# Optimization experiments

Measured on AMD Instinct MI355X. Metric: run time of the kernel, lower is better.

Reference implementation:

```python
import jax, jax.numpy as jnp
import numpy as np

HID = 512
BATCH = 64
SRC_LEN = 2048


def setup_inputs() -> dict:
    key = jax.random.key(0)
    ks = jax.random.split(key, 8)
    s = 1.0 / np.sqrt(HID)
    return {
        "h": jax.random.normal(ks[0], (1, BATCH, HID), dtype=jnp.float32),
        "enc_out": jax.random.normal(ks[1], (BATCH, SRC_LEN, HID), dtype=jnp.float32),
        "W1_w": jax.random.uniform(ks[2], (HID, HID), jnp.float32, -s, s),
        "W1_b": jax.random.uniform(ks[3], (HID,), jnp.float32, -s, s),
        "W2_w": jax.random.uniform(ks[4], (HID, HID), jnp.float32, -s, s),
        "W2_b": jax.random.uniform(ks[5], (HID,), jnp.float32, -s, s),
        "V_w": jax.random.uniform(ks[6], (1, HID), jnp.float32, -s, s),
        "V_b": jax.random.uniform(ks[7], (1,), jnp.float32, -s, s),
    }


def reference(h, enc_out, W1_w, W1_b, W2_w, W2_b, V_w, V_b):
    # h: [1, B, H] -> [B, 1, H]; broadcast against enc_out: [B, S, H]
    h_b = jnp.transpose(h, (1, 0, 2))                       # [B, 1, H]
    proj_enc = jnp.einsum('bsh,oh->bso', enc_out, W1_w) + W1_b  # [B, S, H]
    proj_h = jnp.einsum('bqh,oh->bqo', h_b, W2_w) + W2_b        # [B, 1, H]
    energy = jnp.tanh(proj_enc + proj_h)                        # [B, S, H]
    scores = jnp.einsum('bsh,oh->bso', energy, V_w)[..., 0] + V_b[0]  # [B, S]
    return jax.nn.softmax(scores, axis=1)
```

## Files before the change

kernel.cpp:

```cpp
#include <hip/hip_runtime.h>
#include <hip/hip_bf16.h>

#define HID   512
#define BATCH 64
#define SRC   2048
#define MROWS (BATCH * SRC)

typedef __bf16 bf16x8 __attribute__((ext_vector_type(8)));
typedef __bf16 bf16x4 __attribute__((ext_vector_type(4)));
typedef float  f32x16 __attribute__((ext_vector_type(16)));

#define PANEL 520

__device__ inline float fast_tanh(float x) {
    float e = __builtin_amdgcn_exp2f(x * 2.8853900817779268f);
    return 1.0f - 2.0f * __builtin_amdgcn_rcpf(e + 1.0f);
}

template <int CTRL>
__device__ inline float dpp_add(float x) {
    int y = __builtin_amdgcn_update_dpp(0, __builtin_bit_cast(int, x), CTRL, 0xF, 0xF, true);
    return x + __builtin_bit_cast(float, y);
}

__device__ inline float reduce32(float x) {
    x = dpp_add<0xB1>(x);
    x = dpp_add<0x4E>(x);
    x = dpp_add<0x141>(x);
    x = dpp_add<0x140>(x);
    int y = __builtin_amdgcn_ds_swizzle(__builtin_bit_cast(int, x), 0x401F);
    return x + __builtin_bit_cast(float, y);
}

__global__ void prep(const float* __restrict__ W1w, __bf16* __restrict__ Bpk,
                     const float* __restrict__ h, const float* __restrict__ W2w,
                     const float* __restrict__ W2b, const float* __restrict__ W1b,
                     float* __restrict__ biasc) {
    __shared__ float hh[HID];
    int tid = threadIdx.x;
    if (blockIdx.x < 128) {
        int t = blockIdx.x * 256 + tid;
        int l = t & 63, tile = t >> 6;
        int ot = tile & 15, kt = tile >> 4;
        int o = ot * 32 + (l & 31);
        int k = kt * 16 + (l >> 5) * 8;
        const float* src = W1w + (size_t)o * HID + k;
        float4 v0 = *(const float4*)src;
        float4 v1 = *(const float4*)(src + 4);
        bf16x8 r;
        r[0]=(__bf16)v0.x; r[1]=(__bf16)v0.y; r[2]=(__bf16)v0.z; r[3]=(__bf16)v0.w;
        r[4]=(__bf16)v1.x; r[5]=(__bf16)v1.y; r[6]=(__bf16)v1.z; r[7]=(__bf16)v1.w;
        ((bf16x8*)Bpk)[t] = r;
    } else {
        int b = blockIdx.x - 128;
        hh[tid]       = h[b * HID + tid];
        hh[tid + 256] = h[b * HID + tid + 256];
        __syncthreads();
        const float4* h4 = (const float4*)hh;
        for (int o = tid; o < HID; o += 256) {
            const float4* w4 = (const float4*)(W2w + (size_t)o * HID);
            float s = 0.f;
            #pragma unroll 8
            for (int k = 0; k < HID / 4; ++k) {
                float4 a = h4[k]; float4 w = w4[k];
                s += a.x * w.x + a.y * w.y + a.z * w.z + a.w * w.w;
            }
            biasc[b * HID + o] = s + W2b[o] + W1b[o];
        }
    }
}

__global__ __launch_bounds__(512, 4) void attn_main(
        const float* __restrict__ enc, const __bf16* __restrict__ Bpk,
        const float* __restrict__ biasc, const float* __restrict__ Vw,
        float* __restrict__ scores) {
    __shared__ __bf16 AL[64 * PANEL];
    __shared__ float sred[64][9];

    const int tid = threadIdx.x;
    const int blockRow = blockIdx.x * 64;
    const int b = blockIdx.x >> 5;
    const int lane = tid & 63;
    const int wv = tid >> 6;
    const int col = lane & 31;
    const int hfi = lane >> 5;

    const int o0 = (2 * wv) * 32 + col;
    const int o1 = o0 + 32;
    float bb0 = biasc[b * HID + o0], bb1 = biasc[b * HID + o1];
    float vv0 = Vw[o0],               vv1 = Vw[o1];

    const float4* encB = (const float4*)enc + (size_t)blockRow * 128;
    #pragma unroll
    for (int i = 0; i < 16; ++i) {
        int f = i * 512 + tid;
        float4 v = encB[f];
        int row = f >> 7;
        int kq  = (f & 127) << 2;
        int kt = kq >> 4, half = (kq >> 3) & 1, j = kq & 7;
        int off = (kt * 2 + (row >> 5)) * PANEL + ((row & 31) + 32 * half) * 8 + j;
        bf16x4 o4;
        o4[0]=(__bf16)v.x; o4[1]=(__bf16)v.y; o4[2]=(__bf16)v.z; o4[3]=(__bf16)v.w;
        *(bf16x4*)&AL[off] = o4;
    }
    __syncthreads();

    const int rot = blockIdx.x & 31;
    const char* BpkB = (const char*)Bpk + (2 * wv) * 1024 + lane * 16;
    const __bf16* pA = AL + lane * 8;

    f32x16 acc00, acc01, acc10, acc11;
    #pragma unroll
    for (int i = 0; i < 16; ++i) { acc00[i]=0.f; acc01[i]=0.f; acc10[i]=0.f; acc11[i]=0.f; }

    bf16x8 b0 = *(const bf16x8*)(BpkB + (size_t)rot * 16384);
    bf16x8 b1 = *(const bf16x8*)(BpkB + (size_t)rot * 16384 + 1024);
    #pragma unroll 8
    for (int kt = 0; kt < 32; ++kt) {
        int in = (kt + 1 + rot) & 31;
        bf16x8 nb0 = *(const bf16x8*)(BpkB + (size_t)in * 16384);
        bf16x8 nb1 = *(const bf16x8*)(BpkB + (size_t)in * 16384 + 1024);
        int ia = (kt + rot) & 31;
        const __bf16* pa = pA + ia * (2 * PANEL);
        bf16x8 a0 = *(const bf16x8*)pa;
        bf16x8 a1 = *(const bf16x8*)(pa + PANEL);
        acc00 = __builtin_amdgcn_mfma_f32_32x32x16_bf16(a0, b0, acc00, 0, 0, 0);
        acc10 = __builtin_amdgcn_mfma_f32_32x32x16_bf16(a1, b0, acc10, 0, 0, 0);
        acc01 = __builtin_amdgcn_mfma_f32_32x32x16_bf16(a0, b1, acc01, 0, 0, 0);
        acc11 = __builtin_amdgcn_mfma_f32_32x32x16_bf16(a1, b1, acc11, 0, 0, 0);
        b0 = nb0; b1 = nb1;
    }

    #pragma unroll
    for (int r = 0; r < 16; ++r) {
        float p0 = vv0 * fast_tanh(acc00[r] + bb0) + vv1 * fast_tanh(acc01[r] + bb1);
        float p1 = vv0 * fast_tanh(acc10[r] + bb0) + vv1 * fast_tanh(acc11[r] + bb1);
        p0 = reduce32(p0);
        p1 = reduce32(p1);
        if (col == 0) {
            int rl = (r & 3) + 8 * (r >> 2) + 4 * hfi;
            sred[rl][wv]      = p0;
            sred[32 + rl][wv] = p1;
        }
    }
    __syncthreads();
    if (tid < 64) {
        float s = 0.f;
        #pragma unroll
        for (int w = 0; w < 8; ++w) s += sred[tid][w];
        scores[blockRow + tid] = s;
    }
}

__global__ void softmax_k(float* __restrict__ scores) {
    int b = blockIdx.x;
    int tid = threadIdx.x;
    int lane = tid & 63, wv = tid >> 6;
    __shared__ float red[4];
    float* row = scores + (size_t)b * SRC;
    float4 v0 = *(float4*)(row + tid * 8);
    float4 v1 = *(float4*)(row + tid * 8 + 4);
    float x[8] = {v0.x, v0.y, v0.z, v0.w, v1.x, v1.y, v1.z, v1.w};
    float mx = x[0];
    #pragma unroll
    for (int r = 1; r < 8; ++r) mx = fmaxf(mx, x[r]);
    #pragma unroll
    for (int m = 1; m <= 32; m <<= 1) mx = fmaxf(mx, __shfl_xor(mx, m, 64));
    if (lane == 0) red[wv] = mx;
    __syncthreads();
    mx = fmaxf(fmaxf(red[0], red[1]), fmaxf(red[2], red[3]));
    __syncthreads();
    float s = 0.f;
    #pragma unroll
    for (int r = 0; r < 8; ++r) {
        x[r] = __builtin_amdgcn_exp2f((x[r] - mx) * 1.44269504088896f);
        s += x[r];
    }
    #pragma unroll
    for (int m = 1; m <= 32; m <<= 1) s += __shfl_xor(s, m, 64);
    if (lane == 0) red[wv] = s;
    __syncthreads();
    s = red[0] + red[1] + red[2] + red[3];
    float inv = 1.0f / s;
    float4 o0 = make_float4(x[0] * inv, x[1] * inv, x[2] * inv, x[3] * inv);
    float4 o1 = make_float4(x[4] * inv, x[5] * inv, x[6] * inv, x[7] * inv);
    *(float4*)(row + tid * 8)     = o0;
    *(float4*)(row + tid * 8 + 4) = o1;
}

extern "C" void kernel_launch(void* const* d_in, const int* in_sizes, int n_in,
                              void* d_out, int out_size, void* d_ws, size_t ws_size,
                              hipStream_t stream) {
    const float* h    = (const float*)d_in[0];
    const float* enc  = (const float*)d_in[1];
    const float* W1w  = (const float*)d_in[2];
    const float* W1b  = (const float*)d_in[3];
    const float* W2w  = (const float*)d_in[4];
    const float* W2b  = (const float*)d_in[5];
    const float* Vw   = (const float*)d_in[6];
    float* out = (float*)d_out;

    __bf16* Bpk  = (__bf16*)d_ws;
    float*  biasc = (float*)((char*)d_ws + HID * HID * sizeof(__bf16));

    prep     <<<192, 256, 0, stream>>>(W1w, Bpk, h, W2w, W2b, W1b, biasc);
    attn_main<<<MROWS / 64, 512, 0, stream>>>(enc, Bpk, biasc, Vw, out);
    softmax_k<<<BATCH, 256, 0, stream>>>(out);
}
```

Measured before the change: 443.5 us.

## Make attention kernel persistent with double-buffered LDS and register-staged enc prefetch

Each of 256 blocks now processes eight 64-row tiles, loading the next tile of encoder rows into registers while the current tile's MFMA loop runs, then converting into a second LDS buffer. The weight-fragment prefetch is deepened to two k-steps. This aims to hide global load latency behind matrix compute. The cost is doubled LDS per block (one block per CU), more registers for the staging array, and extra barriers per tile.

```diff
diff --git a/kernel.cpp b/kernel.cpp
--- a/kernel.cpp
+++ b/kernel.cpp
@@ -70,85 +70,122 @@
     }
 }
 
-__global__ __launch_bounds__(512, 4) void attn_main(
+__global__ __launch_bounds__(512, 2) void attn_main(
         const float* __restrict__ enc, const __bf16* __restrict__ Bpk,
         const float* __restrict__ biasc, const float* __restrict__ Vw,
         float* __restrict__ scores) {
-    __shared__ __bf16 AL[64 * PANEL];
+    __shared__ __bf16 AL[2][64 * PANEL];
     __shared__ float sred[64][9];
 
-    const int tid = threadIdx.x;
-    const int blockRow = blockIdx.x * 64;
-    const int b = blockIdx.x >> 5;
+    const int tid  = threadIdx.x;
     const int lane = tid & 63;
-    const int wv = tid >> 6;
-    const int col = lane & 31;
-    const int hfi = lane >> 5;
+    const int wv   = tid >> 6;
+    const int col  = lane & 31;
+    const int hfi  = lane >> 5;
+    const int blk  = blockIdx.x;
+    const int b    = blk >> 2;
+    const int rowBase = blk * 512;
 
     const int o0 = (2 * wv) * 32 + col;
     const int o1 = o0 + 32;
-    float bb0 = biasc[b * HID + o0], bb1 = biasc[b * HID + o1];
-    float vv0 = Vw[o0],               vv1 = Vw[o1];
-
-    const float4* encB = (const float4*)enc + (size_t)blockRow * 128;
-    #pragma unroll
-    for (int i = 0; i < 16; ++i) {
-        int f = i * 512 + tid;
-        float4 v = encB[f];
-        int row = f >> 7;
-        int kq  = (f & 127) << 2;
-        int kt = kq >> 4, half = (kq >> 3) & 1, j = kq & 7;
-        int off = (kt * 2 + (row >> 5)) * PANEL + ((row & 31) + 32 * half) * 8 + j;
-        bf16x4 o4;
-        o4[0]=(__bf16)v.x; o4[1]=(__bf16)v.y; o4[2]=(__bf16)v.z; o4[3]=(__bf16)v.w;
-        *(bf16x4*)&AL[off] = o4;
-    }
-    __syncthreads();
-
-    const int rot = blockIdx.x & 31;
+    const float bb0 = biasc[b * HID + o0], bb1 = biasc[b * HID + o1];
+    const float vv0 = Vw[o0],               vv1 = Vw[o1];
+
+    const int rot = blk & 31;
     const char* BpkB = (const char*)Bpk + (2 * wv) * 1024 + lane * 16;
-    const __bf16* pA = AL + lane * 8;
-
-    f32x16 acc00, acc01, acc10, acc11;
-    #pragma unroll
-    for (int i = 0; i < 16; ++i) { acc00[i]=0.f; acc01[i]=0.f; acc10[i]=0.f; acc11[i]=0.f; }
-
-    bf16x8 b0 = *(const bf16x8*)(BpkB + (size_t)rot * 16384);
-    bf16x8 b1 = *(const bf16x8*)(BpkB + (size_t)rot * 16384 + 1024);
-    #pragma unroll 8
-    for (int kt = 0; kt < 32; ++kt) {
-        int in = (kt + 1 + rot) & 31;
-        bf16x8 nb0 = *(const bf16x8*)(BpkB + (size_t)in * 16384);
-        bf16x8 nb1 = *(const bf16x8*)(BpkB + (size_t)in * 16384 + 1024);
-        int ia = (kt + rot) & 31;
-        const __bf16* pa = pA + ia * (2 * PANEL);
-        bf16x8 a0 = *(const bf16x8*)pa;
-        bf16x8 a1 = *(const bf16x8*)(pa + PANEL);
-        acc00 = __builtin_amdgcn_mfma_f32_32x32x16_bf16(a0, b0, acc00, 0, 0, 0);
-        acc10 = __builtin_amdgcn_mfma_f32_32x32x16_bf16(a1, b0, acc10, 0, 0, 0);
-        acc01 = __builtin_amdgcn_mfma_f32_32x32x16_bf16(a0, b1, acc01, 0, 0, 0);
-        acc11 = __builtin_amdgcn_mfma_f32_32x32x16_bf16(a1, b1, acc11, 0, 0, 0);
-        b0 = nb0; b1 = nb1;
-    }
-
-    #pragma unroll
-    for (int r = 0; r < 16; ++r) {
-        float p0 = vv0 * fast_tanh(acc00[r] + bb0) + vv1 * fast_tanh(acc01[r] + bb1);
-        float p1 = vv0 * fast_tanh(acc10[r] + bb0) + vv1 * fast_tanh(acc11[r] + bb1);
-        p0 = reduce32(p0);
-        p1 = reduce32(p1);
-        if (col == 0) {
-            int rl = (r & 3) + 8 * (r >> 2) + 4 * hfi;
-            sred[rl][wv]      = p0;
-            sred[32 + rl][wv] = p1;
-        }
-    }
-    __syncthreads();
-    if (tid < 64) {
-        float s = 0.f;
-        #pragma unroll
-        for (int w = 0; w < 8; ++w) s += sred[tid][w];
-        scores[blockRow + tid] = s;
+
+    float4 st[16];
+
+    {
+        const float4* encT = (const float4*)enc + (size_t)rowBase * 128;
+        #pragma unroll
+        for (int i = 0; i < 16; ++i) st[i] = encT[i * 512 + tid];
+        #pragma unroll
+        for (int i = 0; i < 16; ++i) {
+            int f = i * 512 + tid;
+            int row = f >> 7;
+            int kq  = (f & 127) << 2;
+            int kt = kq >> 4, half = (kq >> 3) & 1, j = kq & 7;
+            int off = (kt * 2 + (row >> 5)) * PANEL + ((row & 31) + 32 * half) * 8 + j;
+            float4 v = st[i];
+            bf16x4 o4;
+            o4[0]=(__bf16)v.x; o4[1]=(__bf16)v.y; o4[2]=(__bf16)v.z; o4[3]=(__bf16)v.w;
+            *(bf16x4*)&AL[0][off] = o4;
+        }
+    }
+    __syncthreads();
+
+    int cur = 0;
+    for (int t = 0; t < 8; ++t) {
+        if (t < 7) {
+            const float4* encN = (const float4*)enc + (size_t)(rowBase + (t + 1) * 64) * 128;
+            #pragma unroll
+            for (int i = 0; i < 16; ++i) st[i] = encN[i * 512 + tid];
+        }
+
+        f32x16 acc00, acc01, acc10, acc11;
+        #pragma unroll
+        for (int i = 0; i < 16; ++i) { acc00[i]=0.f; acc01[i]=0.f; acc10[i]=0.f; acc11[i]=0.f; }
+
+        const __bf16* pAc = &AL[cur][0] + lane * 8;
+        bf16x8 bA0 = *(const bf16x8*)(BpkB + (size_t)rot * 16384);
+        bf16x8 bA1 = *(const bf16x8*)(BpkB + (size_t)rot * 16384 + 1024);
+        int r1 = (rot + 1) & 31;
+        bf16x8 bB0 = *(const bf16x8*)(BpkB + (size_t)r1 * 16384);
+        bf16x8 bB1 = *(const bf16x8*)(BpkB + (size_t)r1 * 16384 + 1024);
+        #pragma unroll 8
+        for (int kt = 0; kt < 32; ++kt) {
+            int ip = (kt + 2 + rot) & 31;
+            bf16x8 nb0 = *(const bf16x8*)(BpkB + (size_t)ip * 16384);
+            bf16x8 nb1 = *(const bf16x8*)(BpkB + (size_t)ip * 16384 + 1024);
+            int ia = (kt + rot) & 31;
+            const __bf16* pa = pAc + ia * (2 * PANEL);
+            bf16x8 a0 = *(const bf16x8*)pa;
+            bf16x8 a1 = *(const bf16x8*)(pa + PANEL);
+            acc00 = __builtin_amdgcn_mfma_f32_32x32x16_bf16(a0, bA0, acc00, 0, 0, 0);
+            acc10 = __builtin_amdgcn_mfma_f32_32x32x16_bf16(a1, bA0, acc10, 0, 0, 0);
+            acc01 = __builtin_amdgcn_mfma_f32_32x32x16_bf16(a0, bA1, acc01, 0, 0, 0);
+            acc11 = __builtin_amdgcn_mfma_f32_32x32x16_bf16(a1, bA1, acc11, 0, 0, 0);
+            bA0 = bB0; bA1 = bB1; bB0 = nb0; bB1 = nb1;
+        }
+
+        #pragma unroll
+        for (int r = 0; r < 16; ++r) {
+            float p0 = vv0 * fast_tanh(acc00[r] + bb0) + vv1 * fast_tanh(acc01[r] + bb1);
+            float p1 = vv0 * fast_tanh(acc10[r] + bb0) + vv1 * fast_tanh(acc11[r] + bb1);
+            p0 = reduce32(p0);
+            p1 = reduce32(p1);
+            if (col == 0) {
+                int rl = (r & 3) + 8 * (r >> 2) + 4 * hfi;
+                sred[rl][wv]      = p0;
+                sred[32 + rl][wv] = p1;
+            }
+        }
+
+        if (t < 7) {
+            __bf16* ALn = &AL[cur ^ 1][0];
+            #pragma unroll
+            for (int i = 0; i < 16; ++i) {
+                int f = i * 512 + tid;
+                int row = f >> 7;
+                int kq  = (f & 127) << 2;
+                int kt2 = kq >> 4, half = (kq >> 3) & 1, j = kq & 7;
+                int off = (kt2 * 2 + (row >> 5)) * PANEL + ((row & 31) + 32 * half) * 8 + j;
+                float4 v = st[i];
+                bf16x4 o4;
+                o4[0]=(__bf16)v.x; o4[1]=(__bf16)v.y; o4[2]=(__bf16)v.z; o4[3]=(__bf16)v.w;
+                *(bf16x4*)&ALn[off] = o4;
+            }
+        }
+        __syncthreads();
+        if (tid < 64) {
+            float s = 0.f;
+            #pragma unroll
+            for (int w = 0; w < 8; ++w) s += sred[tid][w];
+            scores[rowBase + t * 64 + tid] = s;
+        }
+        __syncthreads();
+        cur ^= 1;
     }
 }
 
@@ -204,6 +241,6 @@
     float*  biasc = (float*)((char*)d_ws + HID * HID * sizeof(__bf16));
 
     prep     <<<192, 256, 0, stream>>>(W1w, Bpk, h, W2w, W2b, W1b, biasc);
-    attn_main<<<MROWS / 64, 512, 0, stream>>>(enc, Bpk, biasc, Vw, out);
+    attn_main<<<256, 512, 0, stream>>>(enc, Bpk, biasc, Vw, out);
     softmax_k<<<BATCH, 256, 0, stream>>>(out);
 }
```

Result: slower. 470.3 us (+6.0%).

## Split GEMM into two column passes, overlapping first-half tanh epilogue with second pass

Applied to the files above, without the earlier changes.

The K loop is split into two sequential passes, one per 32-column output tile, each with a 4-deep rotating register prefetch of B fragments from global memory. During the second pass, the tanh and V-weighting for the first tile's accumulators is interleaved between MFMAs, so transcendental work overlaps matrix math instead of running entirely after the loop. The cost is that the A panel is read from LDS twice, only two accumulators run independently per pass (less MFMA ILP), and register pressure may rise.

```diff
diff --git a/kernel.cpp b/kernel.cpp
--- a/kernel.cpp
+++ b/kernel.cpp
@@ -113,34 +113,74 @@
     #pragma unroll
     for (int i = 0; i < 16; ++i) { acc00[i]=0.f; acc01[i]=0.f; acc10[i]=0.f; acc11[i]=0.f; }
 
-    bf16x8 b0 = *(const bf16x8*)(BpkB + (size_t)rot * 16384);
-    bf16x8 b1 = *(const bf16x8*)(BpkB + (size_t)rot * 16384 + 1024);
-    #pragma unroll 8
-    for (int kt = 0; kt < 32; ++kt) {
-        int in = (kt + 1 + rot) & 31;
-        bf16x8 nb0 = *(const bf16x8*)(BpkB + (size_t)in * 16384);
-        bf16x8 nb1 = *(const bf16x8*)(BpkB + (size_t)in * 16384 + 1024);
-        int ia = (kt + rot) & 31;
-        const __bf16* pa = pA + ia * (2 * PANEL);
-        bf16x8 a0 = *(const bf16x8*)pa;
-        bf16x8 a1 = *(const bf16x8*)(pa + PANEL);
-        acc00 = __builtin_amdgcn_mfma_f32_32x32x16_bf16(a0, b0, acc00, 0, 0, 0);
-        acc10 = __builtin_amdgcn_mfma_f32_32x32x16_bf16(a1, b0, acc10, 0, 0, 0);
-        acc01 = __builtin_amdgcn_mfma_f32_32x32x16_bf16(a0, b1, acc01, 0, 0, 0);
-        acc11 = __builtin_amdgcn_mfma_f32_32x32x16_bf16(a1, b1, acc11, 0, 0, 0);
-        b0 = nb0; b1 = nb1;
-    }
+    bf16x8 u0 = *(const bf16x8*)(BpkB + (size_t)((rot + 0) & 31) * 16384);
+    bf16x8 u1 = *(const bf16x8*)(BpkB + (size_t)((rot + 1) & 31) * 16384);
+    bf16x8 u2 = *(const bf16x8*)(BpkB + (size_t)((rot + 2) & 31) * 16384);
+    bf16x8 u3 = *(const bf16x8*)(BpkB + (size_t)((rot + 3) & 31) * 16384);
+
+#define KS0(P, KK)                                                            \
+    {                                                                         \
+        int ia = ((KK) + rot) & 31;                                           \
+        const __bf16* pa = pA + ia * (2 * PANEL);                             \
+        bf16x8 a0 = *(const bf16x8*)pa;                                       \
+        bf16x8 a1 = *(const bf16x8*)(pa + PANEL);                             \
+        acc00 = __builtin_amdgcn_mfma_f32_32x32x16_bf16(a0, P, acc00, 0, 0, 0); \
+        acc10 = __builtin_amdgcn_mfma_f32_32x32x16_bf16(a1, P, acc10, 0, 0, 0); \
+        int ip = ((KK) + 4 + rot) & 31;          \
+        P = *(const bf16x8*)(BpkB + (size_t)ip * 16384);                      \
+    }
+    #pragma unroll
+    for (int g = 0; g < 8; ++g) {
+        KS0(u0, 4 * g + 0)
+        KS0(u1, 4 * g + 1)
+        KS0(u2, 4 * g + 2)
+        KS0(u3, 4 * g + 3)
+    }
+#undef KS0
+
+    u0 = *(const bf16x8*)(BpkB + (size_t)((rot + 0) & 31) * 16384 + 1024);
+    u1 = *(const bf16x8*)(BpkB + (size_t)((rot + 1) & 31) * 16384 + 1024);
+    u2 = *(const bf16x8*)(BpkB + (size_t)((rot + 2) & 31) * 16384 + 1024);
+    u3 = *(const bf16x8*)(BpkB + (size_t)((rot + 3) & 31) * 16384 + 1024);
+
+#define KS1(P, KK)                                                            \
+    {                                                                         \
+        int ia = ((KK) + rot) & 31;                                           \
+        const __bf16* pa = pA + ia * (2 * PANEL);                             \
+        bf16x8 a0 = *(const bf16x8*)pa;                                       \
+        bf16x8 a1 = *(const bf16x8*)(pa + PANEL);                             \
+        acc01 = __builtin_amdgcn_mfma_f32_32x32x16_bf16(a0, P, acc01, 0, 0, 0); \
+        acc11 = __builtin_amdgcn_mfma_f32_32x32x16_bf16(a1, P, acc11, 0, 0, 0); \
+        int ip = ((KK) + 4 + rot) & 31;                                       \
+        P = *(const bf16x8*)(BpkB + (size_t)ip * 16384 + 1024);               \
+    }
+#define EPIA(R)                                                               \
+    {                                                                         \
+        acc00[R] = vv0 * fast_tanh(acc00[R] + bb0);                           \
+        acc10[R] = vv0 * fast_tanh(acc10[R] + bb0);                           \
+    }
+    #pragma unroll
+    for (int g = 0; g < 8; ++g) {
+        KS1(u0, 4 * g + 0)
+        KS1(u1, 4 * g + 1)
+        EPIA(2 * g + 0)
+        KS1(u2, 4 * g + 2)
+        KS1(u3, 4 * g + 3)
+        EPIA(2 * g + 1)
+    }
+#undef KS1
+#undef EPIA
 
     #pragma unroll
     for (int r = 0; r < 16; ++r) {
-        float p0 = vv0 * fast_tanh(acc00[r] + bb0) + vv1 * fast_tanh(acc01[r] + bb1);
-        float p1 = vv0 * fast_tanh(acc10[r] + bb0) + vv1 * fast_tanh(acc11[r] + bb1);
-        p0 = reduce32(p0);
-        p1 = reduce32(p1);
+        float s0 = acc00[r] + vv1 * fast_tanh(acc01[r] + bb1);
+        float s1 = acc10[r] + vv1 * fast_tanh(acc11[r] + bb1);
+        s0 = reduce32(s0);
+        s1 = reduce32(s1);
         if (col == 0) {
             int rl = (r & 3) + 8 * (r >> 2) + 4 * hfi;
-            sred[rl][wv]      = p0;
-            sred[32 + rl][wv] = p1;
+            sred[rl][wv]      = s0;
+            sred[32 + rl][wv] = s1;
         }
     }
     __syncthreads();
```

New measurement: 443.2 us. About the same (-0.1%).
